# Optimization experiments

Measured on AMD Instinct MI355X. Metric: run time of the kernel, lower is better.

The kernel has to match this reference:

```python
import jax, jax.numpy as jnp
import numpy as np


def setup_inputs() -> dict:
    key = jax.random.key(0)
    k1, k2, k3, k4 = jax.random.split(key, 4)
    N, M, d = 512, 4096, 8
    return {
        "X": jax.random.normal(k1, (N, M), jnp.float32),
        "C_tilde": jax.random.normal(k2, (d, N), jnp.float32),
        "S_tilde": jax.random.normal(k3, (N, d), jnp.float32),
        "tau_tilde": jax.random.normal(k4, (N, d), jnp.float32),
    }


def reference(X, C_tilde, S_tilde, tau_tilde):
    # X: [N, M] real; C_tilde: [d, N]; S_tilde, tau_tilde: [N, d]
    N, M = X.shape
    f = jnp.arange(M, dtype=X.dtype) / M                         # [M]
    # omega[N,d,M] = exp(-2*pi*i * tau[N,d] * f[M])
    phase = tau_tilde[:, :, None] * f                            # [N, d, M] real
    omega = jnp.exp((-2j * jnp.pi) * phase.astype(jnp.complex64))  # [N, d, M] complex64

    X_F = jnp.fft.fft(X)                                         # [N, M] complex64
    X_F_align = X_F[:, None, :] * jnp.conj(omega)                # [N, d, M]

    C = jax.nn.softmax(C_tilde, axis=1).astype(jnp.complex64)    # [d, N]
    A_F = jnp.einsum('dN,NdM->dM', C, X_F_align)                 # [d, M]

    S = jax.nn.softmax(S_tilde, axis=1).astype(jnp.complex64)    # [N, d]
    # S_shift[N,d,M] = S[N,d] * omega[N,d,M]; x = sum_d S_shift * A_F
    x = jnp.einsum('Nd,NdM,dM->NM', S, omega, A_F)               # [N, M] complex64
    return x
```

## Files before the change

### kernel.cpp

```cpp
#include <hip/hip_runtime.h>
#include <math.h>

#define N_ROWS 512
#define M_LEN  4096
#define D_DIM  8
#define NCHUNK 8

__device__ __forceinline__ float2 f2(float x, float y) { return make_float2(x, y); }

static constexpr float TWO_PI = 6.283185307179586476925f;

__global__ __launch_bounds__(256) void softmax_kernel(
    const float* __restrict__ Ct, const float* __restrict__ St,
    float* __restrict__ C, float* __restrict__ S) {
  int b = blockIdx.x, tid = threadIdx.x;
  if (b < D_DIM) {
    __shared__ float red[256];
    const float* row = Ct + b * N_ROWS;
    float v0 = row[tid], v1 = row[tid + 256];
    float mx = fmaxf(v0, v1);
    red[tid] = mx; __syncthreads();
    for (int s = 128; s > 0; s >>= 1) {
      if (tid < s) red[tid] = fmaxf(red[tid], red[tid + s]);
      __syncthreads();
    }
    float m = red[0];
    __syncthreads();
    float e0 = __expf(v0 - m), e1 = __expf(v1 - m);
    red[tid] = e0 + e1; __syncthreads();
    for (int s = 128; s > 0; s >>= 1) {
      if (tid < s) red[tid] += red[tid + s];
      __syncthreads();
    }
    float inv = 1.0f / red[0];
    C[b * N_ROWS + tid]       = e0 * inv;
    C[b * N_ROWS + tid + 256] = e1 * inv;
  } else {
    int n = (b - D_DIM) * 256 + tid;
    if (n < N_ROWS) {
      float v[D_DIM];
      float mx = -3.0e38f;
      #pragma unroll
      for (int d = 0; d < D_DIM; ++d) { v[d] = St[n * D_DIM + d]; mx = fmaxf(mx, v[d]); }
      float sum = 0.f;
      #pragma unroll
      for (int d = 0; d < D_DIM; ++d) { v[d] = __expf(v[d] - mx); sum += v[d]; }
      float inv = 1.0f / sum;
      #pragma unroll
      for (int d = 0; d < D_DIM; ++d) S[n * D_DIM + d] = v[d] * inv;
    }
  }
}

__global__ __launch_bounds__(256) void fft_kernel(
    const float* __restrict__ X, float2* __restrict__ XF) {
  __shared__ float2 buf[M_LEN];
  int row = blockIdx.x;
  int tid = threadIdx.x;
  const float* x = X + (size_t)row * M_LEN;
  for (int j = tid; j < M_LEN; j += 256) {
    int r = (int)(__brev((unsigned)j) >> 20);
    buf[r] = f2(x[j], 0.0f);
  }
  __syncthreads();
  for (int s = 1; s <= 12; ++s) {
    int half = 1 << (s - 1);
    int mlen = 1 << s;
    float base = -TWO_PI / (float)mlen;
    for (int t = tid; t < (M_LEN >> 1); t += 256) {
      int k   = t & (half - 1);
      int grp = t >> (s - 1);
      int i0  = grp * mlen + k;
      int i1  = i0 + half;
      float sw, cw;
      __sincosf(base * (float)k, &sw, &cw);
      float2 a = buf[i0], b = buf[i1];
      float2 wb = f2(cw * b.x - sw * b.y, cw * b.y + sw * b.x);
      buf[i0] = f2(a.x + wb.x, a.y + wb.y);
      buf[i1] = f2(a.x - wb.x, a.y - wb.y);
    }
    __syncthreads();
  }
  for (int j = tid; j < M_LEN; j += 256)
    XF[(size_t)row * M_LEN + j] = buf[j];
}

__global__ __launch_bounds__(256) void zero_af_kernel(float4* __restrict__ AF) {
  int i = blockIdx.x * 256 + threadIdx.x;
  if (i < (D_DIM * M_LEN) / 2)
    AF[i] = make_float4(0.f, 0.f, 0.f, 0.f);
}

__global__ __launch_bounds__(256) void af_kernel(
    const float2* __restrict__ XF, const float* __restrict__ C,
    const float* __restrict__ tau, float* __restrict__ AF) {
  int bid   = blockIdx.x;
  int chunk = bid >> 7;
  int idx   = (bid & 127) * 256 + threadIdx.x;
  int d = idx >> 12;
  int m = idx & (M_LEN - 1);
  float fm = (float)m * (1.0f / (float)M_LEN);
  float accr = 0.f, acci = 0.f;
  int n0 = chunk * (N_ROWS / NCHUNK);
  #pragma unroll 8
  for (int nn = 0; nn < N_ROWS / NCHUNK; ++nn) {
    int n = n0 + nn;
    float c = C[d * N_ROWS + n];
    float t = tau[n * D_DIM + d];
    float sa, ca;
    __sincosf(TWO_PI * t * fm, &sa, &ca);
    float2 Xv = XF[(size_t)n * M_LEN + m];
    accr += c * (Xv.x * ca - Xv.y * sa);
    acci += c * (Xv.x * sa + Xv.y * ca);
  }
  if (idx < D_DIM * M_LEN) {
    atomicAdd(&AF[2 * idx],     accr);
    atomicAdd(&AF[2 * idx + 1], acci);
  }
}

__global__ __launch_bounds__(256) void out_kernel(
    const float2* __restrict__ AF, const float* __restrict__ S,
    const float* __restrict__ tau, float* __restrict__ out, int interleaved) {
  int idx = blockIdx.x * 256 + threadIdx.x;
  int n = idx >> 12;
  int m = idx & (M_LEN - 1);
  float fm = (float)m * (1.0f / (float)M_LEN);
  float xr = 0.f, xi = 0.f;
  #pragma unroll
  for (int d = 0; d < D_DIM; ++d) {
    float s = S[n * D_DIM + d];
    float t = tau[n * D_DIM + d];
    float sa, ca;
    __sincosf(TWO_PI * t * fm, &sa, &ca);
    float2 A = AF[(d << 12) + m];
    xr += s * (ca * A.x + sa * A.y);
    xi += s * (ca * A.y - sa * A.x);
  }
  if (interleaved) {
    ((float2*)out)[idx] = f2(xr, xi);
  } else {
    out[idx] = xr;
  }
}

extern "C" void kernel_launch(void* const* d_in, const int* in_sizes, int n_in,
                              void* d_out, int out_size, void* d_ws, size_t ws_size,
                              hipStream_t stream) {
  const float* X  = (const float*)d_in[0];
  const float* Ct = (const float*)d_in[1];
  const float* St = (const float*)d_in[2];
  const float* tau= (const float*)d_in[3];

  char* ws = (char*)d_ws;
  const size_t XF_BYTES = (size_t)N_ROWS * M_LEN * sizeof(float2);
  const size_t AF_BYTES = (size_t)D_DIM * M_LEN * sizeof(float2);
  const size_t C_BYTES  = (size_t)D_DIM * N_ROWS * sizeof(float);
  float2* XF = (float2*)ws;
  float2* AF = (float2*)(ws + XF_BYTES);
  float*  C  = (float*)(ws + XF_BYTES + AF_BYTES);
  float*  S  = (float*)(ws + XF_BYTES + AF_BYTES + C_BYTES);

  int interleaved = (out_size >= 2 * N_ROWS * M_LEN) ? 1 : 0;

  softmax_kernel<<<D_DIM + (N_ROWS + 255) / 256, 256, 0, stream>>>(Ct, St, C, S);
  fft_kernel<<<N_ROWS, 256, 0, stream>>>(X, XF);
  zero_af_kernel<<<(D_DIM * M_LEN / 2 + 255) / 256, 256, 0, stream>>>((float4*)AF);
  af_kernel<<<NCHUNK * 128, 256, 0, stream>>>(XF, C, tau, (float*)AF);
  out_kernel<<<(N_ROWS * M_LEN) / 256, 256, 0, stream>>>(AF, S, tau, (float*)d_out, interleaved);
}
```

Baseline: 117.1 us.

## Replace radix-2 FFT with radix-4 FFT and padded shared memory

Rewrites the per-row 4096-point FFT from 12 radix-2 stages to 6 radix-4 stages, using digit-reversed input ordering. Shared-memory indices are padded to reduce bank conflicts. This halves the number of barrier-separated passes and the shared-memory round trips, and cuts the twiddle sincos calls. The cost is extra complex multiplies to derive the w2 and w3 twiddles and more index arithmetic per access.

Result: no change. 115.2 us (-1.6%).

```diff
diff --git a/kernel.cpp b/kernel.cpp
--- a/kernel.cpp
+++ b/kernel.cpp
@@ -7,6 +7,18 @@
 #define NCHUNK 8
 
 __device__ __forceinline__ float2 f2(float x, float y) { return make_float2(x, y); }
+__device__ __forceinline__ float2 cmul(float2 a, float2 b){
+  return f2(a.x*b.x - a.y*b.y, a.x*b.y + a.y*b.x);
+}
+__device__ __forceinline__ float2 cadd(float2 a, float2 b){ return f2(a.x+b.x, a.y+b.y); }
+__device__ __forceinline__ float2 csub(float2 a, float2 b){ return f2(a.x-b.x, a.y-b.y); }
+__device__ __forceinline__ int ph(int i){ return i + (i>>4) + (i>>8); }
+__device__ __forceinline__ int dr6(int j){
+  int r = 0;
+  #pragma unroll
+  for (int i = 0; i < 6; ++i){ r = (r<<2) | (j & 3); j >>= 2; }
+  return r;
+}
 
 static constexpr float TWO_PI = 6.283185307179586476925f;
 
@@ -54,35 +66,39 @@
 
 __global__ __launch_bounds__(256) void fft_kernel(
     const float* __restrict__ X, float2* __restrict__ XF) {
-  __shared__ float2 buf[M_LEN];
+  __shared__ float2 buf[4368];
   int row = blockIdx.x;
   int tid = threadIdx.x;
   const float* x = X + (size_t)row * M_LEN;
-  for (int j = tid; j < M_LEN; j += 256) {
-    int r = (int)(__brev((unsigned)j) >> 20);
-    buf[r] = f2(x[j], 0.0f);
-  }
+  for (int j = tid; j < M_LEN; j += 256)
+    buf[ph(dr6(j))] = f2(x[j], 0.0f);
   __syncthreads();
-  for (int s = 1; s <= 12; ++s) {
-    int half = 1 << (s - 1);
-    int mlen = 1 << s;
-    float base = -TWO_PI / (float)mlen;
-    for (int t = tid; t < (M_LEN >> 1); t += 256) {
-      int k   = t & (half - 1);
-      int grp = t >> (s - 1);
-      int i0  = grp * mlen + k;
-      int i1  = i0 + half;
-      float sw, cw;
-      __sincosf(base * (float)k, &sw, &cw);
-      float2 a = buf[i0], b = buf[i1];
-      float2 wb = f2(cw * b.x - sw * b.y, cw * b.y + sw * b.x);
-      buf[i0] = f2(a.x + wb.x, a.y + wb.y);
-      buf[i1] = f2(a.x - wb.x, a.y - wb.y);
+  for (int s = 0; s < 6; ++s) {
+    int quarter = 1 << (2*s);
+    float angf = -TWO_PI / (float)(quarter << 2);
+    for (int bi = tid; bi < 1024; bi += 256) {
+      int k  = bi & (quarter - 1);
+      int g  = bi >> (2*s);
+      int i0 = (g << (2*s + 2)) + k;
+      float sw, cw; __sincosf(angf * (float)k, &sw, &cw);
+      float2 w1 = f2(cw, sw);
+      float2 w2 = cmul(w1, w1);
+      float2 w3 = cmul(w2, w1);
+      float2 a0 = buf[ph(i0)];
+      float2 a1 = cmul(buf[ph(i0 +   quarter)], w1);
+      float2 a2 = cmul(buf[ph(i0 + 2*quarter)], w2);
+      float2 a3 = cmul(buf[ph(i0 + 3*quarter)], w3);
+      float2 t0 = cadd(a0, a2), t1 = csub(a0, a2);
+      float2 t2 = cadd(a1, a3), t3 = csub(a1, a3);
+      buf[ph(i0)]             = cadd(t0, t2);
+      buf[ph(i0 +   quarter)] = f2(t1.x + t3.y, t1.y - t3.x);
+      buf[ph(i0 + 2*quarter)] = csub(t0, t2);
+      buf[ph(i0 + 3*quarter)] = f2(t1.x - t3.y, t1.y + t3.x);
     }
     __syncthreads();
   }
   for (int j = tid; j < M_LEN; j += 256)
-    XF[(size_t)row * M_LEN + j] = buf[j];
+    XF[(size_t)row * M_LEN + j] = buf[ph(j)];
 }
 
 __global__ __launch_bounds__(256) void zero_af_kernel(float4* __restrict__ AF) {
```
